# Kernel optimization log

Hardware: AMD Instinct MI355X
Metric: run time of the kernel (lower is better)

Reference implementation:

```python
import jax, jax.numpy as jnp
import numpy as np

D_IN = 1024
D_OUT = 1024
NUM_HEADS = 16
HEAD_DIM = D_OUT // NUM_HEADS
EPS = 1e-6
POW = 16.0


def setup_inputs() -> dict:
    key = jax.random.key(0)
    ks = jax.random.split(key, 6)
    s = 1.0 / np.sqrt(D_IN)
    x = jax.random.normal(ks[0], (2, 2048, D_IN), dtype=jnp.float32)
    Wq = jax.random.uniform(ks[1], (D_OUT, D_IN), jnp.float32, -s, s)
    Wk = jax.random.uniform(ks[2], (D_OUT, D_IN), jnp.float32, -s, s)
    Wv = jax.random.uniform(ks[3], (D_OUT, D_IN), jnp.float32, -s, s)
    Wo = jax.random.uniform(ks[4], (D_OUT, D_OUT), jnp.float32, -s, s)
    bo = jax.random.uniform(ks[5], (D_OUT,), jnp.float32, -s, s)
    return {"x": x, "Wq": Wq, "Wk": Wk, "Wv": Wv, "Wo": Wo, "bo": bo}


def _l2norm(t):
    # torch F.normalize: t / max(||t||, eps)
    n = jnp.sqrt(jnp.sum(t * t, axis=-1, keepdims=True))
    return t / jnp.maximum(n, EPS)


def reference(x, Wq, Wk, Wv, Wo, bo):
    B, T, _ = x.shape
    # project and split heads: [B, H, T, Dh]
    def heads(W):
        y = jnp.einsum('btd,od->bto', x, W)
        return y.reshape(B, T, NUM_HEADS, HEAD_DIM).transpose(0, 2, 1, 3)
    Q = _l2norm(heads(Wq))
    K = _l2norm(heads(Wk))
    V = heads(Wv)
    cos_sim = jnp.clip(jnp.einsum('bhtd,bhsd->bhts', Q, K), -0.999, 0.999)
    scores = 1.0 - jnp.arccos(cos_sim) / jnp.pi
    W = jnp.power(jnp.maximum(scores, EPS), POW)
    W = W / (jnp.sum(W, axis=-1, keepdims=True) + EPS)
    out = jnp.einsum('bhts,bhsd->bhtd', W, V)
    out = out.transpose(0, 2, 1, 3).reshape(B, T, D_OUT)
    return jnp.einsum('bto,po->btp', out, Wo) + bo
```

## Files before the change

### kernel.cpp

```cpp
#include <hip/hip_runtime.h>
#include <math.h>

constexpr int Dm   = 1024;
constexpr int NH   = 16;
constexpr int HD   = 64;
constexpr int Bb   = 2;
constexpr int Tt   = 2048;
constexpr int MTOT = Bb * Tt;
#define EPSF 1e-6f

typedef __attribute__((ext_vector_type(8))) short short8;
typedef __attribute__((ext_vector_type(4))) float f32x4;
typedef __attribute__((ext_vector_type(16))) float f32x16;
typedef __attribute__((ext_vector_type(2))) float f32x2;

__device__ __forceinline__ ushort f2bf(float f) {
    union { float f; unsigned u; } v; v.f = f;
    unsigned r = (v.u + 0x7FFFu + ((v.u >> 16) & 1u)) >> 16;
    return (ushort)r;
}

__device__ __forceinline__ unsigned cvt_pk_bf16(float lo, float hi) {
    unsigned r;
    asm("v_cvt_pk_bf16_f32 %0, %1, %2" : "=v"(r) : "v"(lo), "v"(hi));
    return r;
}

__device__ __forceinline__ void gload16(const void* g, void* l) {
    __builtin_amdgcn_global_load_lds(
        (const __attribute__((address_space(1))) unsigned int*)g,
        (__attribute__((address_space(3))) unsigned int*)l,
        16, 0, 0);
}

__global__ __launch_bounds__(256)
void cvt_all(const float* __restrict__ x,  const float* __restrict__ wq,
             const float* __restrict__ wk, const float* __restrict__ wv,
             const float* __restrict__ wo,
             ushort* __restrict__ xb,  ushort* __restrict__ wqb,
             ushort* __restrict__ wkb, ushort* __restrict__ wvb,
             ushort* __restrict__ wob) {
    int i = blockIdx.x * 256 + threadIdx.x;
    const float* src; ushort* dst; int off;
    if (i < 1048576)      { src = x;  dst = xb;  off = i; }
    else if (i < 1310720) { src = wq; dst = wqb; off = i - 1048576; }
    else if (i < 1572864) { src = wk; dst = wkb; off = i - 1310720; }
    else if (i < 1835008) { src = wv; dst = wvb; off = i - 1572864; }
    else                  { src = wo; dst = wob; off = i - 1835008; }
    const float4 v = ((const float4*)src)[off];
    ushort4 o;
    o.x = f2bf(v.x); o.y = f2bf(v.y); o.z = f2bf(v.z); o.w = f2bf(v.w);
    ((ushort4*)dst)[off] = o;
}

template<bool OUTF32>
__device__ __forceinline__
void gemm_core(const ushort* __restrict__ A, const ushort* __restrict__ W,
               const float* __restrict__ bias, void* __restrict__ out,
               int m0, int n0, int N, int K, int mode) {
    __shared__ __attribute__((aligned(16))) ushort As[128 * 64];
    __shared__ __attribute__((aligned(16))) ushort Bs[128 * 64];
    const int tid  = threadIdx.x;
    const int wave = tid >> 6, lane = tid & 63;
    const int quad = lane >> 4, l15 = lane & 15;
    const int wr = wave >> 1, wc = wave & 1;
    const int lr = lane >> 3;
    const int sc = (lane & 7) ^ lr;

    f32x4 acc[4][4] = {};
    const ushort* Ab = A + (size_t)(m0 + lr) * K + sc * 8;
    const ushort* Wb = W + (size_t)(n0 + lr) * K + sc * 8;

    for (int k0 = 0; k0 < K; k0 += 64) {
        #pragma unroll
        for (int i = 0; i < 4; i++) {
            const int rows8 = (wave * 4 + i) * 8;
            gload16(Ab + (size_t)rows8 * K + k0, &As[rows8 * 64]);
            gload16(Wb + (size_t)rows8 * K + k0, &Bs[rows8 * 64]);
        }
        __syncthreads();
        #pragma unroll
        for (int kh = 0; kh < 2; kh++) {
            short8 af[4];
            #pragma unroll
            for (int mi = 0; mi < 4; mi++) {
                const int row = wr * 64 + mi * 16 + l15;
                af[mi] = *(const short8*)&As[row * 64 + (((kh * 4 + quad) ^ (row & 7)) * 8)];
            }
            #pragma unroll
            for (int nj = 0; nj < 4; nj++) {
                const int row = wc * 64 + nj * 16 + l15;
                const short8 bf = *(const short8*)&Bs[row * 64 + (((kh * 4 + quad) ^ (row & 7)) * 8)];
                #pragma unroll
                for (int mi = 0; mi < 4; mi++)
                    acc[mi][nj] = __builtin_amdgcn_mfma_f32_16x16x32_bf16(af[mi], bf, acc[mi][nj], 0, 0, 0);
            }
        }
        __syncthreads();
    }

    if (!OUTF32 && mode == 2) {
        ushort* T = (wave < 2 ? As : Bs) + (wave & 1) * 4096;
        const int t_base = m0 + wr * 64;
        const int bb = t_base >> 11, tl = t_base & 2047;
        const int hh = (n0 >> 6) + wc;
        #pragma unroll
        for (int mi = 0; mi < 4; mi++) {
            const int chk = 2 * mi + (quad >> 1);
            #pragma unroll
            for (int nj = 0; nj < 4; nj++) {
                const int dl = nj * 16 + l15;
                const int ch2 = ((chk ^ (dl & 7)) + (dl >> 3)) & 7;
                uint2 pk;
                pk.x = (unsigned)f2bf(acc[mi][nj][0]) | ((unsigned)f2bf(acc[mi][nj][1]) << 16);
                pk.y = (unsigned)f2bf(acc[mi][nj][2]) | ((unsigned)f2bf(acc[mi][nj][3]) << 16);
                *(uint2*)&T[dl * 64 + ch2 * 8 + (quad & 1) * 4] = pk;
            }
        }
        ushort* gp = (ushort*)out + (size_t)((bb * NH + hh) * HD + lane) * Tt + tl;
        #pragma unroll
        for (int c = 0; c < 8; c++) {
            const int ch2 = ((c ^ (lane & 7)) + (lane >> 3)) & 7;
            *(int4*)&gp[c * 8] = *(const int4*)&T[lane * 64 + ch2 * 8];
        }
        return;
    }

    #pragma unroll
    for (int mi = 0; mi < 4; mi++) {
        float inv[4] = {1.f, 1.f, 1.f, 1.f};
        if (!OUTF32 && mode == 1) {
            #pragma unroll
            for (int r = 0; r < 4; r++) {
                float ss = 0.f;
                #pragma unroll
                for (int nj = 0; nj < 4; nj++) ss += acc[mi][nj][r] * acc[mi][nj][r];
                ss += __shfl_xor(ss, 1); ss += __shfl_xor(ss, 2);
                ss += __shfl_xor(ss, 4); ss += __shfl_xor(ss, 8);
                inv[r] = 1.f / fmaxf(sqrtf(ss), EPSF);
            }
        }
        #pragma unroll
        for (int nj = 0; nj < 4; nj++)
            #pragma unroll
            for (int r = 0; r < 4; r++) {
                const int row = m0 + wr * 64 + mi * 16 + quad * 4 + r;
                const int col = n0 + wc * 64 + nj * 16 + l15;
                if (OUTF32)
                    ((float*)out)[(size_t)row * N + col] = acc[mi][nj][r] + bias[col];
                else
                    ((ushort*)out)[(size_t)row * N + col] = f2bf(acc[mi][nj][r] * inv[r]);
            }
    }
}

__global__ __launch_bounds__(256)
void qkv_gemm(const ushort* __restrict__ xb,
              const ushort* __restrict__ wq, const ushort* __restrict__ wk,
              const ushort* __restrict__ wv,
              ushort* __restrict__ qb, ushort* __restrict__ kb,
              ushort* __restrict__ vtb) {
    const int ny = blockIdx.y, sel = ny >> 3;
    const ushort* W = (sel == 0) ? wq : (sel == 1) ? wk : wv;
    ushort* out     = (sel == 0) ? qb : (sel == 1) ? kb : vtb;
    gemm_core<false>(xb, W, nullptr, out, blockIdx.x * 128, (ny & 7) * 128,
                     Dm, Dm, (sel < 2) ? 1 : 2);
}

__global__ __launch_bounds__(256)
void out_gemm(const ushort* __restrict__ A, const ushort* __restrict__ W,
              const float* __restrict__ bias, float* __restrict__ out) {
    __shared__ __attribute__((aligned(16))) ushort As[64 * 64];
    __shared__ __attribute__((aligned(16))) ushort Bs[128 * 64];
    const int tid  = threadIdx.x;
    const int wave = tid >> 6, lane = tid & 63;
    const int quad = lane >> 4, l15 = lane & 15;
    const int wm = wave & 1, wn = wave >> 1;
    const int lr = lane >> 3;
    const int sc = (lane & 7) ^ lr;
    const int m0 = blockIdx.x * 64, n0 = blockIdx.y * 128;
    const int K = Dm, N = Dm;

    f32x4 acc[2][4] = {};
    const ushort* Ab = A + (size_t)(m0 + lr) * K + sc * 8;
    const ushort* Wb = W + (size_t)(n0 + lr) * K + sc * 8;

    for (int k0 = 0; k0 < K; k0 += 64) {
        #pragma unroll
        for (int i = 0; i < 2; i++) {
            const int rows8 = (wave * 2 + i) * 8;
            gload16(Ab + (size_t)rows8 * K + k0, &As[rows8 * 64]);
        }
        #pragma unroll
        for (int i = 0; i < 4; i++) {
            const int rows8 = (wave * 4 + i) * 8;
            gload16(Wb + (size_t)rows8 * K + k0, &Bs[rows8 * 64]);
        }
        __syncthreads();
        #pragma unroll
        for (int kh = 0; kh < 2; kh++) {
            short8 af[2];
            #pragma unroll
            for (int mi = 0; mi < 2; mi++) {
                const int row = wm * 32 + mi * 16 + l15;
                af[mi] = *(const short8*)&As[row * 64 + (((kh * 4 + quad) ^ (row & 7)) * 8)];
            }
            #pragma unroll
            for (int nj = 0; nj < 4; nj++) {
                const int row = wn * 64 + nj * 16 + l15;
                const short8 bf = *(const short8*)&Bs[row * 64 + (((kh * 4 + quad) ^ (row & 7)) * 8)];
                #pragma unroll
                for (int mi = 0; mi < 2; mi++)
                    acc[mi][nj] = __builtin_amdgcn_mfma_f32_16x16x32_bf16(af[mi], bf, acc[mi][nj], 0, 0, 0);
            }
        }
        __syncthreads();
    }
    #pragma unroll
    for (int mi = 0; mi < 2; mi++)
        #pragma unroll
        for (int nj = 0; nj < 4; nj++)
            #pragma unroll
            for (int r = 0; r < 4; r++) {
                const int row = m0 + wm * 32 + mi * 16 + quad * 4 + r;
                const int col = n0 + wn * 64 + nj * 16 + l15;
                out[(size_t)row * N + col] = acc[mi][nj][r] + bias[col];
            }
}

__global__ __launch_bounds__(256, 4)
void attn_kernel(const ushort* __restrict__ Qb, const ushort* __restrict__ Kb,
                 const ushort* __restrict__ Vtb, ushort* __restrict__ Ob) {
    __shared__ __attribute__((aligned(16))) char smem[37120];
    const int tid  = threadIdx.x;
    const int wave = tid >> 6, lane = tid & 63;
    const int s = wave & 1, tm = wave >> 1;
    const int l31 = lane & 31, H = lane >> 5;
    const int t0 = blockIdx.x * 64, h = blockIdx.y, b = blockIdx.z;
    char* tbase = smem + tm * 18432;

    const size_t qrow = (size_t)(b * Tt + t0 + 32 * s + l31) * Dm + h * HD;
    short8 qf[4];
    #pragma unroll
    for (int c = 0; c < 4; c++)
        qf[c] = *(const short8*)&Qb[qrow + 16 * c + 8 * H];

    const int tt = tid & 127;
    const int rk = tt >> 2, ck = (tt & 3) * 2;
    const int rv = tt >> 1, cv = (tt & 1) * 2;
    const size_t kbase  = (size_t)(b * Tt) * Dm + h * HD;
    const size_t vtbase = (size_t)((b * NH + h) * HD) * Tt;
    const ushort* kg = Kb  + kbase  + (size_t)(tm * 1024 + rk) * Dm + ck * 8;
    const ushort* vg = Vtb + vtbase + (size_t)rv * Tt + tm * 1024 + cv * 8;
    const int kw0 = rk * 128 + ((ck ^ (rk & 7)) * 16);
    const int kw1 = rk * 128 + (((ck + 1) ^ (rk & 7)) * 16);
    const int vw0 = rv * 80 + cv * 16;
    const int vw1 = vw0 + 16;

    f32x16 oacc[2] = {};
    f32x2 denp = {0.f, 0.f};

    const f32x2 h3 = { 0.011180f,  0.011180f};
    const f32x2 h2 = {-0.002070f, -0.002070f};
    const f32x2 h1 = { 0.040732f,  0.040732f};
    const f32x2 h0 = { 0.450158f,  0.450158f};

    short8 pk0 = *(const short8*)kg;
    short8 pk1 = *(const short8*)(kg + 8);
    short8 pv0 = *(const short8*)vg;
    short8 pv1 = *(const short8*)(vg + 8);
    *(short8*)(tbase + kw0) = pk0;
    *(short8*)(tbase + kw1) = pk1;
    *(short8*)(tbase + 4096 + vw0) = pv0;
    *(short8*)(tbase + 4096 + vw1) = pv1;
    __syncthreads();

    const ushort* kgp = kg + (size_t)32 * Dm;
    const ushort* vgp = vg + 32;

    for (int i = 0; i < 32; i++) {
        const int p = i & 1;
        const ushort* Kp = (const ushort*)(tbase + p * 9216);
        const ushort* Vp = (const ushort*)(tbase + p * 9216 + 4096);
        if (i < 31) {
            pk0 = *(const short8*)kgp;
            pk1 = *(const short8*)(kgp + 8);
            pv0 = *(const short8*)vgp;
            pv1 = *(const short8*)(vgp + 8);
            kgp += (size_t)32 * Dm;
            vgp += 32;
        }

        f32x16 sf = {};
        #pragma unroll
        for (int c = 0; c < 4; c++) {
            const short8 kf = *(const short8*)&Kp[l31 * 64 + (((2 * c + H) ^ (l31 & 7)) * 8)];
            sf = __builtin_amdgcn_mfma_f32_32x32x16_bf16(kf, qf[c], sf, 0, 0, 0);
        }

        f32x2 w2[8];
        #pragma unroll
        for (int ii = 0; ii < 8; ii++) {
            f32x2 tA;
            tA.x = __builtin_amdgcn_fmed3f(1.0f - sf[2 * ii],     0.001f, 1.999f);
            tA.y = __builtin_amdgcn_fmed3f(1.0f - sf[2 * ii + 1], 0.001f, 1.999f);
            f32x2 pa = __builtin_elementwise_fma(tA, h3, h2);
            pa = __builtin_elementwise_fma(pa, tA, h1);
            pa = __builtin_elementwise_fma(pa, tA, h0);
            f32x2 ra;
            ra.x = __builtin_amdgcn_sqrtf(tA.x); ra.y = __builtin_amdgcn_sqrtf(tA.y);
            const f32x2 one2 = {1.0f, 1.0f};
            f32x2 wa = __builtin_elementwise_fma(-ra, pa, one2);
            wa *= wa; wa *= wa; wa *= wa; wa *= wa;
            denp += wa;
            w2[ii] = wa;
        }

        unsigned P0 = cvt_pk_bf16(w2[0].x, w2[0].y);
        unsigned P1 = cvt_pk_bf16(w2[1].x, w2[1].y);
        unsigned P2 = cvt_pk_bf16(w2[2].x, w2[2].y);
        unsigned P3 = cvt_pk_bf16(w2[3].x, w2[3].y);
        unsigned P4 = cvt_pk_bf16(w2[4].x, w2[4].y);
        unsigned P5 = cvt_pk_bf16(w2[5].x, w2[5].y);
        unsigned P6 = cvt_pk_bf16(w2[6].x, w2[6].y);
        unsigned P7 = cvt_pk_bf16(w2[7].x, w2[7].y);
        asm("v_permlane32_swap_b32 %0, %1" : "+v"(P0), "+v"(P2));
        asm("v_permlane32_swap_b32 %0, %1" : "+v"(P1), "+v"(P3));
        asm("v_permlane32_swap_b32 %0, %1" : "+v"(P4), "+v"(P6));
        asm("v_permlane32_swap_b32 %0, %1" : "+v"(P5), "+v"(P7));
        int4 bi0; bi0.x = (int)P0; bi0.y = (int)P1; bi0.z = (int)P2; bi0.w = (int)P3;
        int4 bi1; bi1.x = (int)P4; bi1.y = (int)P5; bi1.z = (int)P6; bi1.w = (int)P7;
        const short8 B0 = __builtin_bit_cast(short8, bi0);
        const short8 B1 = __builtin_bit_cast(short8, bi1);

        #pragma unroll
        for (int dd = 0; dd < 2; dd++) {
            const int vr = 32 * dd + l31;
            const short8 vf0 = *(const short8*)&Vp[vr * 40 + H * 8];
            const short8 vf1 = *(const short8*)&Vp[vr * 40 + (2 + H) * 8];
            oacc[dd] = __builtin_amdgcn_mfma_f32_32x32x16_bf16(vf0, B0, oacc[dd], 0, 0, 0);
            oacc[dd] = __builtin_amdgcn_mfma_f32_32x32x16_bf16(vf1, B1, oacc[dd], 0, 0, 0);
        }

        if (i < 31) {
            char* nb = tbase + (1 - p) * 9216;
            *(short8*)(nb + kw0) = pk0;
            *(short8*)(nb + kw1) = pk1;
            *(short8*)(nb + 4096 + vw0) = pv0;
            *(short8*)(nb + 4096 + vw1) = pv1;
        }
        __syncthreads();
    }

    float d = denp.x + denp.y;
    d += __shfl_xor(d, 32);

    float* Obuf = (float*)smem;
    float* Den  = (float*)(smem + 36864);
    const int ql = 32 * s + l31;

    if (tm == 1) {
        #pragma unroll
        for (int dd = 0; dd < 2; dd++)
            #pragma unroll
            for (int rg = 0; rg < 16; rg++) {
                const int dloc = 32 * dd + (rg & 3) + 8 * (rg >> 2) + 4 * H;
                Obuf[ql * 65 + dloc] = oacc[dd][rg];
            }
        if (H == 0) Den[ql] = d;
    }
    __syncthreads();

    if (tm == 0) {
        const float inv = __builtin_amdgcn_rcpf(d + Den[ql] + EPSF);
        const size_t orow = (size_t)(b * Tt + t0 + ql) * Dm + h * HD;
        #pragma unroll
        for (int dd = 0; dd < 2; dd++)
            #pragma unroll
            for (int g = 0; g < 4; g++) {
                const int dbase = 32 * dd + 8 * g + 4 * H;
                const float o0 = (oacc[dd][4 * g + 0] + Obuf[ql * 65 + dbase + 0]) * inv;
                const float o1 = (oacc[dd][4 * g + 1] + Obuf[ql * 65 + dbase + 1]) * inv;
                const float o2 = (oacc[dd][4 * g + 2] + Obuf[ql * 65 + dbase + 2]) * inv;
                const float o3 = (oacc[dd][4 * g + 3] + Obuf[ql * 65 + dbase + 3]) * inv;
                uint2 pk2;
                pk2.x = cvt_pk_bf16(o0, o1);
                pk2.y = cvt_pk_bf16(o2, o3);
                *(uint2*)&Ob[orow + dbase] = pk2;
            }
    }
}

extern "C" void kernel_launch(void* const* d_in, const int* in_sizes, int n_in,
                              void* d_out, int out_size, void* d_ws, size_t ws_size,
                              hipStream_t stream) {
    const float* x  = (const float*)d_in[0];
    const float* Wq = (const float*)d_in[1];
    const float* Wk = (const float*)d_in[2];
    const float* Wv = (const float*)d_in[3];
    const float* Wo = (const float*)d_in[4];
    const float* bo = (const float*)d_in[5];
    float* out = (float*)d_out;

    ushort* ws = (ushort*)d_ws;
    const size_t M1 = 1u << 20;
    ushort* xb  = ws;
    ushort* wqb = ws + 4 * M1;
    ushort* wkb = ws + 5 * M1;
    ushort* wvb = ws + 6 * M1;
    ushort* wob = ws + 7 * M1;
    ushort* qb  = ws + 8 * M1;
    ushort* kb  = ws + 12 * M1;
    ushort* vtb = ws + 16 * M1;
    ushort* aob = ws + 20 * M1;

    cvt_all<<<8192, 256, 0, stream>>>(x, Wq, Wk, Wv, Wo, xb, wqb, wkb, wvb, wob);
    qkv_gemm<<<dim3(MTOT / 128, 24), 256, 0, stream>>>(xb, wqb, wkb, wvb, qb, kb, vtb);
    attn_kernel<<<dim3(Tt / 64, NH, Bb), 256, 0, stream>>>(qb, kb, vtb, aob);
    out_gemm<<<dim3(MTOT / 64, Dm / 128), 256, 0, stream>>>(aob, wob, bo, out);
}
```

Before: 216.7 us.

## Double-buffer LDS tiles with BK=32 in QKV and output GEMMs

Both GEMM main loops switch from a single 64-wide K tile to two 32-wide LDS buffers. The next tile's global-to-LDS load is issued before computing on the current one, so memory latency can overlap the MFMA work. The XOR swizzle is redone for the 32-wide rows. This halves the K work per iteration and leaves twice as many iterations and barriers, and correctness depends on the async load completing before the barrier.

```diff
diff --git a/kernel.cpp b/kernel.cpp
--- a/kernel.cpp
+++ b/kernel.cpp
@@ -58,43 +58,54 @@
 void gemm_core(const ushort* __restrict__ A, const ushort* __restrict__ W,
                const float* __restrict__ bias, void* __restrict__ out,
                int m0, int n0, int N, int K, int mode) {
-    __shared__ __attribute__((aligned(16))) ushort As[128 * 64];
-    __shared__ __attribute__((aligned(16))) ushort Bs[128 * 64];
+    __shared__ __attribute__((aligned(16))) ushort As[2 * 128 * 32];
+    __shared__ __attribute__((aligned(16))) ushort Bs[2 * 128 * 32];
     const int tid  = threadIdx.x;
     const int wave = tid >> 6, lane = tid & 63;
     const int quad = lane >> 4, l15 = lane & 15;
     const int wr = wave >> 1, wc = wave & 1;
-    const int lr = lane >> 3;
-    const int sc = (lane & 7) ^ lr;
+
+    const int arow = lane >> 2;
+    const int acs  = (lane & 3) ^ ((arow >> 1) & 3);
+    const ushort* Ag = A + (size_t)(m0 + arow) * K + acs * 8;
+    const ushort* Wg = W + (size_t)(n0 + arow) * K + acs * 8;
+    const int pr = (l15 >> 1) & 3;
 
     f32x4 acc[4][4] = {};
-    const ushort* Ab = A + (size_t)(m0 + lr) * K + sc * 8;
-    const ushort* Wb = W + (size_t)(n0 + lr) * K + sc * 8;
-
-    for (int k0 = 0; k0 < K; k0 += 64) {
-        #pragma unroll
-        for (int i = 0; i < 4; i++) {
-            const int rows8 = (wave * 4 + i) * 8;
-            gload16(Ab + (size_t)rows8 * K + k0, &As[rows8 * 64]);
-            gload16(Wb + (size_t)rows8 * K + k0, &Bs[rows8 * 64]);
-        }
-        __syncthreads();
-        #pragma unroll
-        for (int kh = 0; kh < 2; kh++) {
-            short8 af[4];
-            #pragma unroll
-            for (int mi = 0; mi < 4; mi++) {
-                const int row = wr * 64 + mi * 16 + l15;
-                af[mi] = *(const short8*)&As[row * 64 + (((kh * 4 + quad) ^ (row & 7)) * 8)];
-            }
-            #pragma unroll
-            for (int nj = 0; nj < 4; nj++) {
-                const int row = wc * 64 + nj * 16 + l15;
-                const short8 bf = *(const short8*)&Bs[row * 64 + (((kh * 4 + quad) ^ (row & 7)) * 8)];
-                #pragma unroll
-                for (int mi = 0; mi < 4; mi++)
-                    acc[mi][nj] = __builtin_amdgcn_mfma_f32_16x16x32_bf16(af[mi], bf, acc[mi][nj], 0, 0, 0);
-            }
+
+    #pragma unroll
+    for (int j = 0; j < 2; j++) {
+        const int r16 = wave * 2 + j;
+        gload16(Ag + (size_t)(r16 * 16) * K, &As[r16 * 512]);
+        gload16(Wg + (size_t)(r16 * 16) * K, &Bs[r16 * 512]);
+    }
+    __syncthreads();
+
+    for (int it = 0; it < 32; ++it) {
+        const int cur = (it & 1) * 4096;
+        if (it < 31) {
+            const int nxt = 4096 - cur;
+            const size_t k0 = (size_t)(it + 1) * 32;
+            #pragma unroll
+            for (int j = 0; j < 2; j++) {
+                const int r16 = wave * 2 + j;
+                gload16(Ag + (size_t)(r16 * 16) * K + k0, &As[nxt + r16 * 512]);
+                gload16(Wg + (size_t)(r16 * 16) * K + k0, &Bs[nxt + r16 * 512]);
+            }
+        }
+        short8 af[4];
+        #pragma unroll
+        for (int mi = 0; mi < 4; mi++) {
+            const int row = wr * 64 + mi * 16 + l15;
+            af[mi] = *(const short8*)&As[cur + row * 32 + ((quad ^ pr) * 8)];
+        }
+        #pragma unroll
+        for (int nj = 0; nj < 4; nj++) {
+            const int row = wc * 64 + nj * 16 + l15;
+            const short8 bf = *(const short8*)&Bs[cur + row * 32 + ((quad ^ pr) * 8)];
+            #pragma unroll
+            for (int mi = 0; mi < 4; mi++)
+                acc[mi][nj] = __builtin_amdgcn_mfma_f32_16x16x32_bf16(af[mi], bf, acc[mi][nj], 0, 0, 0);
         }
         __syncthreads();
     }
@@ -170,49 +181,56 @@
 __global__ __launch_bounds__(256)
 void out_gemm(const ushort* __restrict__ A, const ushort* __restrict__ W,
               const float* __restrict__ bias, float* __restrict__ out) {
-    __shared__ __attribute__((aligned(16))) ushort As[64 * 64];
-    __shared__ __attribute__((aligned(16))) ushort Bs[128 * 64];
+    __shared__ __attribute__((aligned(16))) ushort As[2 * 64 * 32];
+    __shared__ __attribute__((aligned(16))) ushort Bs[2 * 128 * 32];
     const int tid  = threadIdx.x;
     const int wave = tid >> 6, lane = tid & 63;
     const int quad = lane >> 4, l15 = lane & 15;
     const int wm = wave & 1, wn = wave >> 1;
-    const int lr = lane >> 3;
-    const int sc = (lane & 7) ^ lr;
     const int m0 = blockIdx.x * 64, n0 = blockIdx.y * 128;
     const int K = Dm, N = Dm;
 
+    const int arow = lane >> 2;
+    const int acs  = (lane & 3) ^ ((arow >> 1) & 3);
+    const ushort* Ag = A + (size_t)(m0 + arow) * K + acs * 8;
+    const ushort* Wg = W + (size_t)(n0 + arow) * K + acs * 8;
+    const int pr = (l15 >> 1) & 3;
+
     f32x4 acc[2][4] = {};
-    const ushort* Ab = A + (size_t)(m0 + lr) * K + sc * 8;
-    const ushort* Wb = W + (size_t)(n0 + lr) * K + sc * 8;
-
-    for (int k0 = 0; k0 < K; k0 += 64) {
-        #pragma unroll
-        for (int i = 0; i < 2; i++) {
-            const int rows8 = (wave * 2 + i) * 8;
-            gload16(Ab + (size_t)rows8 * K + k0, &As[rows8 * 64]);
-        }
-        #pragma unroll
-        for (int i = 0; i < 4; i++) {
-            const int rows8 = (wave * 4 + i) * 8;
-            gload16(Wb + (size_t)rows8 * K + k0, &Bs[rows8 * 64]);
-        }
-        __syncthreads();
-        #pragma unroll
-        for (int kh = 0; kh < 2; kh++) {
-            short8 af[2];
-            #pragma unroll
-            for (int mi = 0; mi < 2; mi++) {
-                const int row = wm * 32 + mi * 16 + l15;
-                af[mi] = *(const short8*)&As[row * 64 + (((kh * 4 + quad) ^ (row & 7)) * 8)];
-            }
-            #pragma unroll
-            for (int nj = 0; nj < 4; nj++) {
-                const int row = wn * 64 + nj * 16 + l15;
-                const short8 bf = *(const short8*)&Bs[row * 64 + (((kh * 4 + quad) ^ (row & 7)) * 8)];
-                #pragma unroll
-                for (int mi = 0; mi < 2; mi++)
-                    acc[mi][nj] = __builtin_amdgcn_mfma_f32_16x16x32_bf16(af[mi], bf, acc[mi][nj], 0, 0, 0);
-            }
+
+    gload16(Ag + (size_t)(wave * 16) * K, &As[wave * 512]);
+    #pragma unroll
+    for (int j = 0; j < 2; j++) {
+        const int r16 = wave * 2 + j;
+        gload16(Wg + (size_t)(r16 * 16) * K, &Bs[r16 * 512]);
+    }
+    __syncthreads();
+
+    for (int it = 0; it < 32; ++it) {
+        const int curA = (it & 1) * 2048, curB = (it & 1) * 4096;
+        if (it < 31) {
+            const int nxtA = 2048 - curA, nxtB = 4096 - curB;
+            const size_t k0 = (size_t)(it + 1) * 32;
+            gload16(Ag + (size_t)(wave * 16) * K + k0, &As[nxtA + wave * 512]);
+            #pragma unroll
+            for (int j = 0; j < 2; j++) {
+                const int r16 = wave * 2 + j;
+                gload16(Wg + (size_t)(r16 * 16) * K + k0, &Bs[nxtB + r16 * 512]);
+            }
+        }
+        short8 af[2];
+        #pragma unroll
+        for (int mi = 0; mi < 2; mi++) {
+            const int row = wm * 32 + mi * 16 + l15;
+            af[mi] = *(const short8*)&As[curA + row * 32 + ((quad ^ pr) * 8)];
+        }
+        #pragma unroll
+        for (int nj = 0; nj < 4; nj++) {
+            const int row = wn * 64 + nj * 16 + l15;
+            const short8 bf = *(const short8*)&Bs[curB + row * 32 + ((quad ^ pr) * 8)];
+            #pragma unroll
+            for (int mi = 0; mi < 2; mi++)
+                acc[mi][nj] = __builtin_amdgcn_mfma_f32_16x16x32_bf16(af[mi], bf, acc[mi][nj], 0, 0, 0);
         }
         __syncthreads();
     }
```

Measured after the change: 214.9 us. Within noise of the previous version (-0.8%).
